# Kernel tuning notes

Hardware: AMD Instinct MI355X
Metric: run time of the kernel (lower is better)

Reference implementation:

```python
import jax, jax.numpy as jnp
import numpy as np

B, D, NUM_HOP, NUM_REL = 8192, 512, 8, 2000  # batch, input_dim, num_hop, num_relation
TAU = 1.0


def setup_inputs() -> dict:
    key = jax.random.key(0)
    ks = jax.random.split(key, 7)
    s = 1.0 / np.sqrt(D)  # PyTorch GRU uniform init bound
    return {
        "query": jax.random.normal(ks[0], (B, D), jnp.float32),
        "W_ih": jax.random.uniform(ks[1], (3 * D, D), jnp.float32, -s, s),
        "W_hh": jax.random.uniform(ks[2], (3 * D, D), jnp.float32, -s, s),
        "b_ih": jax.random.uniform(ks[3], (3 * D,), jnp.float32, -s, s),
        "b_hh": jax.random.uniform(ks[4], (3 * D,), jnp.float32, -s, s),
        "relation": jax.random.normal(ks[5], (2 * NUM_REL, D), jnp.float32),
        "eos": jax.random.normal(ks[6], (1, D), jnp.float32),
    }


def gru_cell(x, h, W_ih, W_hh, b_ih, b_hh):
    # PyTorch nn.GRU cell, gate order (r, z, n)
    gi = x @ W_ih.T + b_ih  # [B, 3D]
    gh = h @ W_hh.T + b_hh  # [B, 3D]
    ir, iz, i_n = jnp.split(gi, 3, axis=-1)
    hr, hz, h_n = jnp.split(gh, 3, axis=-1)
    r = jax.nn.sigmoid(ir + hr)
    z = jax.nn.sigmoid(iz + hz)
    n = jnp.tanh(i_n + r * h_n)
    return (1.0 - z) * n + z * h


def reference(query, W_ih, W_hh, b_ih, b_hh, relation, eos):
    # gru over seq [query, eos] starting from h0 = 0; hidden[1:] == final hx for 1 layer
    h0 = jnp.zeros_like(query)
    h1 = gru_cell(query, h0, W_ih, W_hh, b_ih, b_hh)
    hidden = gru_cell(jnp.broadcast_to(eos, query.shape), h1, W_ih, W_hh, b_ih, b_hh)

    def step(h, _):
        score = jnp.einsum('bd,rd->br', h, relation)          # [B, 2R]
        attention = jax.nn.softmax(score / TAU, axis=-1)
        subgoal = jnp.einsum('br,rd->bd', attention, relation)  # [B, D]
        h_new = gru_cell(subgoal, h, W_ih, W_hh, b_ih, b_hh)
        return h_new, subgoal

    _, subgoals = jax.lax.scan(step, hidden, None, length=NUM_HOP)  # [NUM_HOP, B, D]
    subgoals = jnp.moveaxis(subgoals, 0, 1)  # [B, NUM_HOP, D]
    masks = jnp.ones(subgoals.shape[:-1], dtype=bool)
    return subgoals, masks
```

## Files before the change

### kernel.cpp

```cpp
#include <hip/hip_runtime.h>


typedef _Float16 f16;
typedef _Float16 f16x8 __attribute__((ext_vector_type(8)));
typedef _Float16 f16x4 __attribute__((ext_vector_type(4)));
typedef float    f32x4 __attribute__((ext_vector_type(4)));

constexpr int BATCH = 8192;
constexpr int DDIM  = 512;
constexpr int D3    = 1536;
constexpr int NRELT = 4000;
constexpr int NRELP = 4096;
constexpr int NHOP  = 8;

#define MFMA16(a,b,c) __builtin_amdgcn_mfma_f32_16x16x32_f16((a),(b),(c),0,0,0)

__device__ __forceinline__ void gll16(const void* g, void* l) {
  __builtin_amdgcn_global_load_lds(
      (const __attribute__((address_space(1))) unsigned int*)g,
      (__attribute__((address_space(3))) unsigned int*)l, 16, 0, 0);
}

__global__ __launch_bounds__(256) void k_split(const float* __restrict__ src,
                                               f16* __restrict__ hi, f16* __restrict__ lo, int n) {
  int i = blockIdx.x * 256 + threadIdx.x;
  if (i >= n) return;
  float v = src[i];
  f16 h = (f16)v;
  hi[i] = h;
  lo[i] = (f16)(v - (float)h);
}

__global__ __launch_bounds__(256) void k_prep_rel(const float* __restrict__ rel,
    f16* __restrict__ rhi, f16* __restrict__ rlo,
    f16* __restrict__ thi, f16* __restrict__ tlo) {
  int i = blockIdx.x * 256 + threadIdx.x;
  if (i >= NRELP * DDIM) return;
  int r = i >> 9, d = i & 511;
  float v = (r < NRELT) ? rel[i] : 0.f;
  f16 h = (f16)v, l = (f16)(v - (float)h);
  rhi[i] = h; rlo[i] = l;
  thi[(size_t)d * NRELP + r] = h;
  tlo[(size_t)d * NRELP + r] = l;
}

__global__ __launch_bounds__(64) void k_gieos(const float* __restrict__ W,
                                              const float* __restrict__ eos,
                                              float* __restrict__ out) {
  int o = blockIdx.x;
  float s = 0.f;
  for (int i = threadIdx.x; i < DDIM; i += 64) s += W[(size_t)o * DDIM + i] * eos[i];
  for (int off = 32; off; off >>= 1) s += __shfl_xor(s, off);
  if (threadIdx.x == 0) out[o] = s;
}

template<bool AFROMS, int EPI>
__global__ __launch_bounds__(256, 2)
void gemm_k(const f16* __restrict__ Ahi, const f16* __restrict__ Alo, int lda,
            const f16* __restrict__ Bhi, const f16* __restrict__ Blo, int ldb,
            float* __restrict__ Cout, int ldc, int nbound, int K,
            const float* __restrict__ S, const float* __restrict__ rowm,
            const float* __restrict__ rowil,
            float* __restrict__ outp, f16* __restrict__ shi, f16* __restrict__ slo,
            int hop)
{
  __shared__ f16 lAh[128][32];
  __shared__ f16 lAl[128][32];
  __shared__ f16 lBh[128][32];
  __shared__ f16 lBl[128][32];

  const int tid  = threadIdx.x;
  const int lane = tid & 63;
  const int wave = tid >> 6;
  const int wm = wave >> 1;
  const int wn = wave & 1;
  const int m0 = blockIdx.x * 128;
  const int n0 = blockIdx.y * 128;
  const int rb = lane & 15;
  const int ko = (lane >> 4) * 8;

  f32x4 acc[4][4] = {};

  for (int k0 = 0; k0 < K; k0 += 32) {
    #pragma unroll
    for (int c = 0; c < 2; ++c) {
      const int ch = wave + c * 4;
      const int r  = ch * 16 + (lane >> 2);
      const size_t goff = (size_t)(n0 + r) * ldb + k0 + (lane & 3) * 8;
      gll16(Bhi + goff, &lBh[ch * 16][0]);
      gll16(Blo + goff, &lBl[ch * 16][0]);
    }
    if constexpr (!AFROMS) {
      #pragma unroll
      for (int c = 0; c < 2; ++c) {
        const int ch = wave + c * 4;
        const int r  = ch * 16 + (lane >> 2);
        const size_t goff = (size_t)(m0 + r) * lda + k0 + (lane & 3) * 8;
        gll16(Ahi + goff, &lAh[ch * 16][0]);
        gll16(Alo + goff, &lAl[ch * 16][0]);
      }
    } else {
      #pragma unroll
      for (int it = 0; it < 4; ++it) {
        const int cid = tid + it * 256;
        const int row = cid >> 3;
        const int c4  = (cid & 7) * 4;
        const int kg  = k0 + c4;
        const int gr  = m0 + row;
        f32x4 s4 = *(const f32x4*)(S + (size_t)gr * NRELP + kg);
        const float mr = rowm[gr];
        const float il = rowil[gr];
        f16x4 vh, vl;
        #pragma unroll
        for (int j = 0; j < 4; ++j) {
          float pv = (kg + j < NRELT) ? __expf(s4[j] - mr) * il : 0.f;
          f16 ph = (f16)pv;
          vh[j] = ph;
          vl[j] = (f16)(pv - (float)ph);
        }
        *(f16x4*)&lAh[row][c4] = vh;
        *(f16x4*)&lAl[row][c4] = vl;
      }
    }
    __syncthreads();

    f16x8 ah[4], al[4], bh[4], bl[4];
    #pragma unroll
    for (int f = 0; f < 4; ++f) {
      ah[f] = *(const f16x8*)&lAh[wm * 64 + f * 16 + rb][ko];
      al[f] = *(const f16x8*)&lAl[wm * 64 + f * 16 + rb][ko];
      bh[f] = *(const f16x8*)&lBh[wn * 64 + f * 16 + rb][ko];
      bl[f] = *(const f16x8*)&lBl[wn * 64 + f * 16 + rb][ko];
    }
    #pragma unroll
    for (int fm = 0; fm < 4; ++fm)
      #pragma unroll
      for (int fn = 0; fn < 4; ++fn) {
        acc[fm][fn] = MFMA16(ah[fm], bh[fn], acc[fm][fn]);
        acc[fm][fn] = MFMA16(ah[fm], bl[fn], acc[fm][fn]);
        acc[fm][fn] = MFMA16(al[fm], bh[fn], acc[fm][fn]);
      }
    __syncthreads();
  }

  #pragma unroll
  for (int fm = 0; fm < 4; ++fm)
    #pragma unroll
    for (int fn = 0; fn < 4; ++fn)
      #pragma unroll
      for (int r = 0; r < 4; ++r) {
        const int gr = m0 + wm * 64 + fm * 16 + (lane >> 4) * 4 + r;
        const int gc = n0 + wn * 64 + fn * 16 + rb;
        const float v = acc[fm][fn][r];
        if (gc < nbound) {
          if constexpr (EPI == 0) {
            Cout[(size_t)gr * ldc + gc] = v;
          } else {
            outp[(size_t)gr * (NHOP * DDIM) + (size_t)hop * DDIM + gc] = v;
            const f16 ph = (f16)v;
            shi[(size_t)gr * DDIM + gc] = ph;
            slo[(size_t)gr * DDIM + gc] = (f16)(v - (float)ph);
          }
        }
      }
}

__global__ __launch_bounds__(256)
void k_rowstat(const float* __restrict__ S, float* __restrict__ rowm,
               float* __restrict__ rowil) {
  const int row = blockIdx.x;
  const float* p = S + (size_t)row * NRELP;
  const int tid = threadIdx.x, lane = tid & 63, wv = tid >> 6;
  __shared__ float redm[4], reds[4];
  float mx = -3.402823e38f;
  for (int c = tid; c < NRELT / 4; c += 256) {
    f32x4 v = *(const f32x4*)(p + c * 4);
    mx = fmaxf(fmaxf(fmaxf(mx, v[0]), fmaxf(v[1], v[2])), v[3]);
  }
  for (int o = 32; o; o >>= 1) mx = fmaxf(mx, __shfl_xor(mx, o));
  if (lane == 0) redm[wv] = mx;
  __syncthreads();
  mx = fmaxf(fmaxf(redm[0], redm[1]), fmaxf(redm[2], redm[3]));
  float s = 0.f;
  for (int c = tid; c < NRELT / 4; c += 256) {
    f32x4 v = *(const f32x4*)(p + c * 4);
    s += __expf(v[0] - mx) + __expf(v[1] - mx) + __expf(v[2] - mx) + __expf(v[3] - mx);
  }
  for (int o = 32; o; o >>= 1) s += __shfl_xor(s, o);
  if (lane == 0) reds[wv] = s;
  __syncthreads();
  if (tid == 0) {
    rowm[row]  = mx;
    rowil[row] = 1.f / (reds[0] + reds[1] + reds[2] + reds[3]);
  }
}

__global__ __launch_bounds__(256)
void k_gates(const float* __restrict__ gi, const float* __restrict__ givec,
             const float* __restrict__ gh,
             const float* __restrict__ bih, const float* __restrict__ bhh,
             const float* __restrict__ hin, float* __restrict__ hout,
             f16* __restrict__ hhi, f16* __restrict__ hlo)
{
  const int idx = blockIdx.x * 256 + threadIdx.x;
  const int b  = idx >> 7;
  const int d4 = (idx & 127) * 4;
  f32x4 ir, iz, inn;
  if (gi) {
    const float* g = gi + (size_t)b * D3 + d4;
    ir  = *(const f32x4*)(g);
    iz  = *(const f32x4*)(g + DDIM);
    inn = *(const f32x4*)(g + 2 * DDIM);
  } else {
    ir  = *(const f32x4*)(givec + d4);
    iz  = *(const f32x4*)(givec + DDIM + d4);
    inn = *(const f32x4*)(givec + 2 * DDIM + d4);
  }
  ir  += *(const f32x4*)(bih + d4);
  iz  += *(const f32x4*)(bih + DDIM + d4);
  inn += *(const f32x4*)(bih + 2 * DDIM + d4);
  f32x4 hr = {0.f, 0.f, 0.f, 0.f}, hz = {0.f, 0.f, 0.f, 0.f}, hn = {0.f, 0.f, 0.f, 0.f};
  if (gh) {
    const float* g = gh + (size_t)b * D3 + d4;
    hr = *(const f32x4*)(g);
    hz = *(const f32x4*)(g + DDIM);
    hn = *(const f32x4*)(g + 2 * DDIM);
  }
  hr += *(const f32x4*)(bhh + d4);
  hz += *(const f32x4*)(bhh + DDIM + d4);
  hn += *(const f32x4*)(bhh + 2 * DDIM + d4);
  f32x4 hp = {0.f, 0.f, 0.f, 0.f};
  if (hin) hp = *(const f32x4*)(hin + (size_t)b * DDIM + d4);
  f32x4 hv; f16x4 vh, vl;
  #pragma unroll
  for (int j = 0; j < 4; ++j) {
    const float r = 1.f / (1.f + __expf(-(ir[j] + hr[j])));
    const float z = 1.f / (1.f + __expf(-(iz[j] + hz[j])));
    const float n = tanhf(inn[j] + r * hn[j]);
    const float h = (1.f - z) * n + z * hp[j];
    hv[j] = h;
    const f16 ph = (f16)h;
    vh[j] = ph;
    vl[j] = (f16)(h - (float)ph);
  }
  *(f32x4*)(hout + (size_t)b * DDIM + d4) = hv;
  *(f16x4*)(hhi + (size_t)b * DDIM + d4) = vh;
  *(f16x4*)(hlo + (size_t)b * DDIM + d4) = vl;
}

__global__ __launch_bounds__(256) void k_ones(float* __restrict__ o, int n) {
  int i = blockIdx.x * 256 + threadIdx.x;
  if (i < n) o[i] = 1.0f;
}

extern "C" void kernel_launch(void* const* d_in, const int* in_sizes, int n_in,
                              void* d_out, int out_size, void* d_ws, size_t ws_size,
                              hipStream_t stream)
{
  const float* query = (const float*)d_in[0];
  const float* W_ih  = (const float*)d_in[1];
  const float* W_hh  = (const float*)d_in[2];
  const float* b_ih  = (const float*)d_in[3];
  const float* b_hh  = (const float*)d_in[4];
  const float* rel   = (const float*)d_in[5];
  const float* eos   = (const float*)d_in[6];
  float* out = (float*)d_out;
  (void)in_sizes; (void)n_in; (void)out_size; (void)ws_size;

  char* w = (char*)d_ws;
  float* Sb    = (float*)w; w += (size_t)BATCH * NRELP * 4;
  float* hbuf  = (float*)w; w += (size_t)BATCH * DDIM * 4;
  f16* h_hi    = (f16*)w;   w += (size_t)BATCH * DDIM * 2;
  f16* h_lo    = (f16*)w;   w += (size_t)BATCH * DDIM * 2;
  f16* x_hi    = (f16*)w;   w += (size_t)BATCH * DDIM * 2;
  f16* x_lo    = (f16*)w;   w += (size_t)BATCH * DDIM * 2;
  f16* wih_hi  = (f16*)w;   w += (size_t)D3 * DDIM * 2;
  f16* wih_lo  = (f16*)w;   w += (size_t)D3 * DDIM * 2;
  f16* whh_hi  = (f16*)w;   w += (size_t)D3 * DDIM * 2;
  f16* whh_lo  = (f16*)w;   w += (size_t)D3 * DDIM * 2;
  f16* rel_hi  = (f16*)w;   w += (size_t)NRELP * DDIM * 2;
  f16* rel_lo  = (f16*)w;   w += (size_t)NRELP * DDIM * 2;
  f16* relT_hi = (f16*)w;   w += (size_t)DDIM * NRELP * 2;
  f16* relT_lo = (f16*)w;   w += (size_t)DDIM * NRELP * 2;
  float* rowm  = (float*)w; w += (size_t)BATCH * 4;
  float* rowil = (float*)w; w += (size_t)BATCH * 4;
  float* gieos = (float*)w; w += (size_t)D3 * 4;
  float* gi = Sb;
  float* gh = Sb + (size_t)BATCH * D3;

  k_split<<<(BATCH * DDIM + 255) / 256, 256, 0, stream>>>(query, x_hi, x_lo, BATCH * DDIM);
  k_split<<<(D3 * DDIM + 255) / 256, 256, 0, stream>>>(W_ih, wih_hi, wih_lo, D3 * DDIM);
  k_split<<<(D3 * DDIM + 255) / 256, 256, 0, stream>>>(W_hh, whh_hi, whh_lo, D3 * DDIM);
  k_prep_rel<<<(NRELP * DDIM + 255) / 256, 256, 0, stream>>>(rel, rel_hi, rel_lo, relT_hi, relT_lo);
  k_gieos<<<D3, 64, 0, stream>>>(W_ih, eos, gieos);

  const int ggrid = BATCH * DDIM / 4 / 256;

  gemm_k<false, 0><<<dim3(64, 12), 256, 0, stream>>>(x_hi, x_lo, DDIM, wih_hi, wih_lo, DDIM,
      gi, D3, D3, DDIM, nullptr, nullptr, nullptr, nullptr, nullptr, nullptr, 0);
  k_gates<<<ggrid, 256, 0, stream>>>(gi, nullptr, nullptr, b_ih, b_hh, nullptr, hbuf, h_hi, h_lo);

  gemm_k<false, 0><<<dim3(64, 12), 256, 0, stream>>>(h_hi, h_lo, DDIM, whh_hi, whh_lo, DDIM,
      gh, D3, D3, DDIM, nullptr, nullptr, nullptr, nullptr, nullptr, nullptr, 0);
  k_gates<<<ggrid, 256, 0, stream>>>(nullptr, gieos, gh, b_ih, b_hh, hbuf, hbuf, h_hi, h_lo);

  for (int hop = 0; hop < NHOP; ++hop) {
    gemm_k<false, 0><<<dim3(64, 32), 256, 0, stream>>>(h_hi, h_lo, DDIM, rel_hi, rel_lo, DDIM,
        Sb, NRELP, NRELT, DDIM, nullptr, nullptr, nullptr, nullptr, nullptr, nullptr, 0);
    k_rowstat<<<BATCH, 256, 0, stream>>>(Sb, rowm, rowil);
    gemm_k<true, 1><<<dim3(64, 4), 256, 0, stream>>>(nullptr, nullptr, 0, relT_hi, relT_lo, NRELP,
        nullptr, 0, DDIM, NRELP, Sb, rowm, rowil, out, x_hi, x_lo, hop);
    gemm_k<false, 0><<<dim3(64, 12), 256, 0, stream>>>(x_hi, x_lo, DDIM, wih_hi, wih_lo, DDIM,
        gi, D3, D3, DDIM, nullptr, nullptr, nullptr, nullptr, nullptr, nullptr, 0);
    gemm_k<false, 0><<<dim3(64, 12), 256, 0, stream>>>(h_hi, h_lo, DDIM, whh_hi, whh_lo, DDIM,
        gh, D3, D3, DDIM, nullptr, nullptr, nullptr, nullptr, nullptr, nullptr, 0);
    k_gates<<<ggrid, 256, 0, stream>>>(gi, nullptr, gh, b_ih, b_hh, hbuf, hbuf, h_hi, h_lo);
  }

  k_ones<<<(BATCH * NHOP + 255) / 256, 256, 0, stream>>>(out + (size_t)BATCH * NHOP * DDIM, BATCH * NHOP);
}
```

Measured before the change: 3.509 ms.

## Store scores as split fp16, fuse softmax into one pass, split-K attention GEMM

The score GEMM now writes hi/lo fp16 pairs instead of fp32. A single-pass online-softmax kernel normalizes the scores in place and writes the probabilities back as hi/lo fp16. The attention×relation GEMM now reads those precomputed probabilities through the async LDS-load path and splits K four ways across blockIdx.z, then a reduction kernel sums the partials and writes the outputs. The aim is to halve score traffic, drop the second softmax read pass and the per-tile exp recompute, and raise occupancy for the 64x4-grid GEMM. The cost is an extra 4×B×D fp32 partial buffer and one more reduction kernel per hop.

```diff
diff --git a/kernel.cpp b/kernel.cpp
--- a/kernel.cpp
+++ b/kernel.cpp
@@ -54,15 +54,12 @@
   if (threadIdx.x == 0) out[o] = s;
 }
 
-template<bool AFROMS, int EPI>
+template<int EPI>
 __global__ __launch_bounds__(256, 2)
 void gemm_k(const f16* __restrict__ Ahi, const f16* __restrict__ Alo, int lda,
             const f16* __restrict__ Bhi, const f16* __restrict__ Blo, int ldb,
-            float* __restrict__ Cout, int ldc, int nbound, int K,
-            const float* __restrict__ S, const float* __restrict__ rowm,
-            const float* __restrict__ rowil,
-            float* __restrict__ outp, f16* __restrict__ shi, f16* __restrict__ slo,
-            int hop)
+            float* __restrict__ Cout, f16* __restrict__ Chi, f16* __restrict__ Clo,
+            int ldc, int K)
 {
   __shared__ f16 lAh[128][32];
   __shared__ f16 lAl[128][32];
@@ -79,9 +76,12 @@
   const int rb = lane & 15;
   const int ko = (lane >> 4) * 8;
 
+  const int kst = blockIdx.z * K;
+  Cout += (size_t)blockIdx.z * (size_t)gridDim.x * 128 * (size_t)ldc;
+
   f32x4 acc[4][4] = {};
 
-  for (int k0 = 0; k0 < K; k0 += 32) {
+  for (int k0 = kst; k0 < kst + K; k0 += 32) {
     #pragma unroll
     for (int c = 0; c < 2; ++c) {
       const int ch = wave + c * 4;
@@ -90,37 +90,13 @@
       gll16(Bhi + goff, &lBh[ch * 16][0]);
       gll16(Blo + goff, &lBl[ch * 16][0]);
     }
-    if constexpr (!AFROMS) {
-      #pragma unroll
-      for (int c = 0; c < 2; ++c) {
-        const int ch = wave + c * 4;
-        const int r  = ch * 16 + (lane >> 2);
-        const size_t goff = (size_t)(m0 + r) * lda + k0 + (lane & 3) * 8;
-        gll16(Ahi + goff, &lAh[ch * 16][0]);
-        gll16(Alo + goff, &lAl[ch * 16][0]);
-      }
-    } else {
-      #pragma unroll
-      for (int it = 0; it < 4; ++it) {
-        const int cid = tid + it * 256;
-        const int row = cid >> 3;
-        const int c4  = (cid & 7) * 4;
-        const int kg  = k0 + c4;
-        const int gr  = m0 + row;
-        f32x4 s4 = *(const f32x4*)(S + (size_t)gr * NRELP + kg);
-        const float mr = rowm[gr];
-        const float il = rowil[gr];
-        f16x4 vh, vl;
-        #pragma unroll
-        for (int j = 0; j < 4; ++j) {
-          float pv = (kg + j < NRELT) ? __expf(s4[j] - mr) * il : 0.f;
-          f16 ph = (f16)pv;
-          vh[j] = ph;
-          vl[j] = (f16)(pv - (float)ph);
-        }
-        *(f16x4*)&lAh[row][c4] = vh;
-        *(f16x4*)&lAl[row][c4] = vl;
-      }
+    #pragma unroll
+    for (int c = 0; c < 2; ++c) {
+      const int ch = wave + c * 4;
+      const int r  = ch * 16 + (lane >> 2);
+      const size_t goff = (size_t)(m0 + r) * lda + k0 + (lane & 3) * 8;
+      gll16(Ahi + goff, &lAh[ch * 16][0]);
+      gll16(Alo + goff, &lAl[ch * 16][0]);
     }
     __syncthreads();
 
@@ -152,47 +128,95 @@
         const int gr = m0 + wm * 64 + fm * 16 + (lane >> 4) * 4 + r;
         const int gc = n0 + wn * 64 + fn * 16 + rb;
         const float v = acc[fm][fn][r];
-        if (gc < nbound) {
-          if constexpr (EPI == 0) {
-            Cout[(size_t)gr * ldc + gc] = v;
-          } else {
-            outp[(size_t)gr * (NHOP * DDIM) + (size_t)hop * DDIM + gc] = v;
-            const f16 ph = (f16)v;
-            shi[(size_t)gr * DDIM + gc] = ph;
-            slo[(size_t)gr * DDIM + gc] = (f16)(v - (float)ph);
-          }
+        if constexpr (EPI == 0) {
+          Cout[(size_t)gr * ldc + gc] = v;
+        } else {
+          const f16 vh = (f16)v;
+          Chi[(size_t)gr * ldc + gc] = vh;
+          Clo[(size_t)gr * ldc + gc] = (f16)(v - (float)vh);
         }
       }
 }
 
 __global__ __launch_bounds__(256)
-void k_rowstat(const float* __restrict__ S, float* __restrict__ rowm,
-               float* __restrict__ rowil) {
+void k_softmax(f16* __restrict__ Shi, f16* __restrict__ Slo) {
   const int row = blockIdx.x;
-  const float* p = S + (size_t)row * NRELP;
+  f16* phi = Shi + (size_t)row * NRELP;
+  f16* plo = Slo + (size_t)row * NRELP;
   const int tid = threadIdx.x, lane = tid & 63, wv = tid >> 6;
-  __shared__ float redm[4], reds[4];
+  const int ng = (tid < 232) ? 4 : 3;
+  f32x4 v[4];
   float mx = -3.402823e38f;
-  for (int c = tid; c < NRELT / 4; c += 256) {
-    f32x4 v = *(const f32x4*)(p + c * 4);
-    mx = fmaxf(fmaxf(fmaxf(mx, v[0]), fmaxf(v[1], v[2])), v[3]);
-  }
-  for (int o = 32; o; o >>= 1) mx = fmaxf(mx, __shfl_xor(mx, o));
-  if (lane == 0) redm[wv] = mx;
+  #pragma unroll
+  for (int i = 0; i < 4; ++i)
+    if (i < ng) {
+      f16x4 hv = *(const f16x4*)(phi + (tid + 256 * i) * 4);
+      f16x4 lv = *(const f16x4*)(plo + (tid + 256 * i) * 4);
+      #pragma unroll
+      for (int j = 0; j < 4; ++j) v[i][j] = (float)hv[j] + (float)lv[j];
+      mx = fmaxf(fmaxf(fmaxf(mx, v[i][0]), fmaxf(v[i][1], v[i][2])), v[i][3]);
+    }
+  float l = 0.f;
+  #pragma unroll
+  for (int i = 0; i < 4; ++i)
+    if (i < ng)
+      l += __expf(v[i][0] - mx) + __expf(v[i][1] - mx)
+         + __expf(v[i][2] - mx) + __expf(v[i][3] - mx);
+  #pragma unroll
+  for (int off = 1; off < 64; off <<= 1) {
+    float om = __shfl_xor(mx, off), ol = __shfl_xor(l, off);
+    float nm = fmaxf(mx, om);
+    l = l * __expf(mx - nm) + ol * __expf(om - nm);
+    mx = nm;
+  }
+  __shared__ float sm[4], sl[4];
+  if (lane == 0) { sm[wv] = mx; sl[wv] = l; }
   __syncthreads();
-  mx = fmaxf(fmaxf(redm[0], redm[1]), fmaxf(redm[2], redm[3]));
-  float s = 0.f;
-  for (int c = tid; c < NRELT / 4; c += 256) {
-    f32x4 v = *(const f32x4*)(p + c * 4);
-    s += __expf(v[0] - mx) + __expf(v[1] - mx) + __expf(v[2] - mx) + __expf(v[3] - mx);
-  }
-  for (int o = 32; o; o >>= 1) s += __shfl_xor(s, o);
-  if (lane == 0) reds[wv] = s;
-  __syncthreads();
-  if (tid == 0) {
-    rowm[row]  = mx;
-    rowil[row] = 1.f / (reds[0] + reds[1] + reds[2] + reds[3]);
-  }
+  const float fm = fmaxf(fmaxf(sm[0], sm[1]), fmaxf(sm[2], sm[3]));
+  const float fl = sl[0] * __expf(sm[0] - fm) + sl[1] * __expf(sm[1] - fm)
+                 + sl[2] * __expf(sm[2] - fm) + sl[3] * __expf(sm[3] - fm);
+  const float il = 1.f / fl;
+  #pragma unroll
+  for (int i = 0; i < 4; ++i)
+    if (i < ng) {
+      f16x4 oh, ol;
+      #pragma unroll
+      for (int j = 0; j < 4; ++j) {
+        const float pv = __expf(v[i][j] - fm) * il;
+        const f16 ph = (f16)pv;
+        oh[j] = ph;
+        ol[j] = (f16)(pv - (float)ph);
+      }
+      *(f16x4*)(phi + (tid + 256 * i) * 4) = oh;
+      *(f16x4*)(plo + (tid + 256 * i) * 4) = ol;
+    }
+  if (tid < 24) {
+    f16x4 z = {(f16)0.f, (f16)0.f, (f16)0.f, (f16)0.f};
+    *(f16x4*)(phi + (1000 + tid) * 4) = z;
+    *(f16x4*)(plo + (1000 + tid) * 4) = z;
+  }
+}
+
+__global__ __launch_bounds__(256)
+void k_subred(const float* __restrict__ Cp, float* __restrict__ outp,
+              f16* __restrict__ xhi, f16* __restrict__ xlo, int hop) {
+  const int idx = blockIdx.x * 256 + threadIdx.x;
+  const int b = idx >> 7, d4 = (idx & 127) * 4;
+  const size_t o = (size_t)b * DDIM + d4;
+  f32x4 s = *(const f32x4*)(Cp + o);
+  s += *(const f32x4*)(Cp + (size_t)BATCH * DDIM + o);
+  s += *(const f32x4*)(Cp + 2 * (size_t)BATCH * DDIM + o);
+  s += *(const f32x4*)(Cp + 3 * (size_t)BATCH * DDIM + o);
+  *(f32x4*)(outp + (size_t)b * (NHOP * DDIM) + (size_t)hop * DDIM + d4) = s;
+  f16x4 vh, vl;
+  #pragma unroll
+  for (int j = 0; j < 4; ++j) {
+    const f16 ph = (f16)s[j];
+    vh[j] = ph;
+    vl[j] = (f16)(s[j] - (float)ph);
+  }
+  *(f16x4*)(xhi + o) = vh;
+  *(f16x4*)(xlo + o) = vl;
 }
 
 __global__ __launch_bounds__(256)
@@ -268,7 +292,9 @@
   (void)in_sizes; (void)n_in; (void)out_size; (void)ws_size;
 
   char* w = (char*)d_ws;
-  float* Sb    = (float*)w; w += (size_t)BATCH * NRELP * 4;
+  f16* SPhi    = (f16*)w;   w += (size_t)BATCH * NRELP * 2;
+  f16* SPlo    = (f16*)w;   w += (size_t)BATCH * NRELP * 2;
+  float* Cpart = (float*)w; w += (size_t)4 * BATCH * DDIM * 4;
   float* hbuf  = (float*)w; w += (size_t)BATCH * DDIM * 4;
   f16* h_hi    = (f16*)w;   w += (size_t)BATCH * DDIM * 2;
   f16* h_lo    = (f16*)w;   w += (size_t)BATCH * DDIM * 2;
@@ -282,11 +308,9 @@
   f16* rel_lo  = (f16*)w;   w += (size_t)NRELP * DDIM * 2;
   f16* relT_hi = (f16*)w;   w += (size_t)DDIM * NRELP * 2;
   f16* relT_lo = (f16*)w;   w += (size_t)DDIM * NRELP * 2;
-  float* rowm  = (float*)w; w += (size_t)BATCH * 4;
-  float* rowil = (float*)w; w += (size_t)BATCH * 4;
   float* gieos = (float*)w; w += (size_t)D3 * 4;
-  float* gi = Sb;
-  float* gh = Sb + (size_t)BATCH * D3;
+  float* gi = (float*)SPhi;
+  float* gh = (float*)SPhi + (size_t)BATCH * D3;
 
   k_split<<<(BATCH * DDIM + 255) / 256, 256, 0, stream>>>(query, x_hi, x_lo, BATCH * DDIM);
   k_split<<<(D3 * DDIM + 255) / 256, 256, 0, stream>>>(W_ih, wih_hi, wih_lo, D3 * DDIM);
@@ -296,24 +320,25 @@
 
   const int ggrid = BATCH * DDIM / 4 / 256;
 
-  gemm_k<false, 0><<<dim3(64, 12), 256, 0, stream>>>(x_hi, x_lo, DDIM, wih_hi, wih_lo, DDIM,
-      gi, D3, D3, DDIM, nullptr, nullptr, nullptr, nullptr, nullptr, nullptr, 0);
+  gemm_k<0><<<dim3(64, 12), 256, 0, stream>>>(x_hi, x_lo, DDIM, wih_hi, wih_lo, DDIM,
+      gi, nullptr, nullptr, D3, DDIM);
   k_gates<<<ggrid, 256, 0, stream>>>(gi, nullptr, nullptr, b_ih, b_hh, nullptr, hbuf, h_hi, h_lo);
 
-  gemm_k<false, 0><<<dim3(64, 12), 256, 0, stream>>>(h_hi, h_lo, DDIM, whh_hi, whh_lo, DDIM,
-      gh, D3, D3, DDIM, nullptr, nullptr, nullptr, nullptr, nullptr, nullptr, 0);
+  gemm_k<0><<<dim3(64, 12), 256, 0, stream>>>(h_hi, h_lo, DDIM, whh_hi, whh_lo, DDIM,
+      gh, nullptr, nullptr, D3, DDIM);
   k_gates<<<ggrid, 256, 0, stream>>>(nullptr, gieos, gh, b_ih, b_hh, hbuf, hbuf, h_hi, h_lo);
 
   for (int hop = 0; hop < NHOP; ++hop) {
-    gemm_k<false, 0><<<dim3(64, 32), 256, 0, stream>>>(h_hi, h_lo, DDIM, rel_hi, rel_lo, DDIM,
-        Sb, NRELP, NRELT, DDIM, nullptr, nullptr, nullptr, nullptr, nullptr, nullptr, 0);
-    k_rowstat<<<BATCH, 256, 0, stream>>>(Sb, rowm, rowil);
-    gemm_k<true, 1><<<dim3(64, 4), 256, 0, stream>>>(nullptr, nullptr, 0, relT_hi, relT_lo, NRELP,
-        nullptr, 0, DDIM, NRELP, Sb, rowm, rowil, out, x_hi, x_lo, hop);
-    gemm_k<false, 0><<<dim3(64, 12), 256, 0, stream>>>(x_hi, x_lo, DDIM, wih_hi, wih_lo, DDIM,
-        gi, D3, D3, DDIM, nullptr, nullptr, nullptr, nullptr, nullptr, nullptr, 0);
-    gemm_k<false, 0><<<dim3(64, 12), 256, 0, stream>>>(h_hi, h_lo, DDIM, whh_hi, whh_lo, DDIM,
-        gh, D3, D3, DDIM, nullptr, nullptr, nullptr, nullptr, nullptr, nullptr, 0);
+    gemm_k<1><<<dim3(64, 32), 256, 0, stream>>>(h_hi, h_lo, DDIM, rel_hi, rel_lo, DDIM,
+        nullptr, SPhi, SPlo, NRELP, DDIM);
+    k_softmax<<<BATCH, 256, 0, stream>>>(SPhi, SPlo);
+    gemm_k<0><<<dim3(64, 4, 4), 256, 0, stream>>>(SPhi, SPlo, NRELP,
+        relT_hi, relT_lo, NRELP, Cpart, nullptr, nullptr, DDIM, NRELP / 4);
+    k_subred<<<ggrid, 256, 0, stream>>>(Cpart, out, x_hi, x_lo, hop);
+    gemm_k<0><<<dim3(64, 12), 256, 0, stream>>>(x_hi, x_lo, DDIM, wih_hi, wih_lo, DDIM,
+        gi, nullptr, nullptr, D3, DDIM);
+    gemm_k<0><<<dim3(64, 12), 256, 0, stream>>>(h_hi, h_lo, DDIM, whh_hi, whh_lo, DDIM,
+        gh, nullptr, nullptr, D3, DDIM);
     k_gates<<<ggrid, 256, 0, stream>>>(gi, nullptr, gh, b_ih, b_hh, hbuf, hbuf, h_hi, h_lo);
   }
 
```

New measurement: 3.300 ms. -5.9%, faster.
